# Kernel tuning notes

Measured on AMD Instinct MI355X. Metric: run time of the kernel, lower is better.

## Reference

```python
import jax, jax.numpy as jnp
import numpy as np

B, N = 1, 768
C_S, C_Z, C_H, H, P_QK, P_V = 384, 128, 16, 12, 4, 8
INF = 100000.0
EPS = 1e-8


def _points(s, w, b, rot, trans, P):
    # PointProjection: linear -> [B,N,H,3,P] -> [B,N,H,P,3] local points,
    # then global = R @ p_local + t (rigid broadcast over heads/points).
    pl = (s @ w + b).reshape(s.shape[0], s.shape[1], H, 3, P)
    pl = jnp.moveaxis(pl, -2, -1)  # [B,N,H,P,3]
    return jnp.einsum('bnij,bnhpj->bnhpi', rot, pl) + trans[:, :, None, None, :]


def setup_inputs():
    key = jax.random.key(0)
    ks = jax.random.split(key, 14)

    def lin(k, fi, fo):
        k1, k2 = jax.random.split(k)
        w = jax.random.normal(k1, (fi, fo), jnp.float32) / np.float32(np.sqrt(fi))
        b = jax.random.normal(k2, (fo,), jnp.float32) * 0.01
        return w, b

    s = jax.random.normal(ks[0], (B, N, C_S), jnp.float32)
    z = jax.random.normal(ks[1], (B, N, N, C_Z), jnp.float32)
    rot = jnp.linalg.qr(jax.random.normal(ks[2], (B, N, 3, 3), jnp.float32))[0]
    trans = jax.random.normal(ks[3], (B, N, 3), jnp.float32)
    mask = jnp.ones((B, N), jnp.float32)

    w_q, b_q = lin(ks[4], C_S, H * C_H)
    w_k, b_k = lin(ks[5], C_S, H * C_H)
    w_v, b_v = lin(ks[6], C_S, H * C_H)
    w_qp, b_qp = lin(ks[7], C_S, H * 3 * P_QK)
    w_kp, b_kp = lin(ks[8], C_S, H * 3 * P_QK)
    w_vp, b_vp = lin(ks[9], C_S, H * 3 * P_V)
    w_b, b_b = lin(ks[10], C_Z, H)
    head_weights = jax.random.normal(ks[11], (H,), jnp.float32) * 0.1
    w_o, b_o = lin(ks[12], H * (C_Z + C_H + 4 * P_V), C_S)

    return dict(s=s, z=z, rot=rot, trans=trans, mask=mask,
                w_q=w_q, b_q=b_q, w_k=w_k, b_k=b_k, w_v=w_v, b_v=b_v,
                w_qp=w_qp, b_qp=b_qp, w_kp=w_kp, b_kp=b_kp, w_vp=w_vp, b_vp=b_vp,
                w_b=w_b, b_b=b_b, head_weights=head_weights, w_o=w_o, b_o=b_o)


def reference(s, z, rot, trans, mask,
              w_q, b_q, w_k, b_k, w_v, b_v,
              w_qp, b_qp, w_kp, b_kp, w_vp, b_vp,
              w_b, b_b, head_weights, w_o, b_o):
    # per-head point weights: sqrt(2 / (9 * P_QK)) * softplus(head_weights)
    pw = np.float32(np.sqrt(2.0 / (9.0 * P_QK))) * jnp.logaddexp(head_weights, 0.0)  # [H]

    q_pts = _points(s, w_qp, b_qp, rot, trans, P_QK)  # [B,N,H,P,3]
    k_pts = _points(s, w_kp, b_kp, rot, trans, P_QK)

    # sum_p ||q_p - k_p||^2 expanded: |q|^2 + |k|^2 - 2 q.k (summed over p,xyz)
    qk_pt = jnp.einsum('bqhpc,bkhpc->bqkh', q_pts, k_pts)
    q2 = jnp.sum(q_pts * q_pts, axis=(-2, -1))  # [B,N,H]
    k2 = jnp.sum(k_pts * k_pts, axis=(-2, -1))
    pt_att = -0.5 * pw * (q2[:, :, None, :] + k2[:, None, :, :] - 2.0 * qk_pt)  # [B,Nq,Nk,H]

    q = (s @ w_q + b_q).reshape(B, N, H, C_H) * np.float32(np.sqrt(1.0 / C_H))
    k = (s @ w_k + b_k).reshape(B, N, H, C_H)
    a = pt_att + jnp.einsum('bqhc,bkhc->bqkh', q, k)
    a = a + (z @ w_b + b_b)  # pair bias [B,Nq,Nk,H]

    sq_mask = mask[:, :, None] * mask[:, None, :]
    a = a + (INF * (sq_mask - 1.0))[..., None]
    a = jax.nn.softmax(a * np.float32(np.sqrt(1.0 / 3.0)), axis=-2)  # softmax over k

    v = (s @ w_v + b_v).reshape(B, N, H, C_H)
    o = jnp.einsum('bqkh,bkhc->bqhc', a, v).reshape(B, N, H * C_H)

    v_pts = _points(s, w_vp, b_vp, rot, trans, P_V)  # [B,N,H,P,3]
    o_pt = jnp.einsum('bqkh,bkhpc->bqhpc', a, v_pts).reshape(B, N, H * P_V, 3)
    # inverse rigid: R^T @ (p - t)
    o_pt = jnp.einsum('bnji,bnpj->bnpi', rot, o_pt - trans[:, :, None, :])  # [B,N,H*P_V,3]
    o_pt_norm = jnp.sqrt(jnp.sum(o_pt * o_pt, axis=-1) + EPS)  # [B,N,H*P_V]

    o_pair = jnp.einsum('bqkh,bqkc->bqhc', a, z).reshape(B, N, H * C_Z)

    cat = jnp.concatenate(
        [o, o_pt[..., 0], o_pt[..., 1], o_pt[..., 2], o_pt_norm, o_pair], axis=-1)
    return cat @ w_o + b_o  # [B,N,C_S]
```

## Files before the change

kernel.cpp:

```cpp
#include <hip/hip_runtime.h>
#include <math.h>

#define NN 768
#define KALL 1152
#define CATD 2112
#define INF_ 100000.0f

__device__ __forceinline__ float4 ld4(const float* p) { return *(const float4*)p; }

__global__ __launch_bounds__(256) void pack_kernel(
    const float* wq, const float* bq, const float* wk, const float* bk,
    const float* wv, const float* bv, const float* wqp, const float* bqp,
    const float* wkp, const float* bkp, const float* wvp, const float* bvp,
    float* Wall, float* ball) {
  int idx = blockIdx.x * 256 + threadIdx.x;
  if (idx >= 385 * KALL) return;
  int kk = idx / KALL, u = idx - kk * KALL;
  const float *w, *b; int col, dim; float sc = 1.f;
  if (u < 192)      { w = wq;  b = bq;  col = u;       dim = 192; sc = 0.25f; }
  else if (u < 384) { w = wk;  b = bk;  col = u - 192; dim = 192; }
  else if (u < 576) { w = wv;  b = bv;  col = u - 384; dim = 192; }
  else if (u < 720) { w = wqp; b = bqp; col = u - 576; dim = 144; }
  else if (u < 864) { w = wkp; b = bkp; col = u - 720; dim = 144; }
  else              { w = wvp; b = bvp; col = u - 864; dim = 288; }
  if (kk < 384) Wall[kk * KALL + u] = sc * w[kk * dim + col];
  else          ball[u] = sc * b[col];
}

__global__ __launch_bounds__(256) void proj_kernel(const float* s, const float* Wall,
                                                   const float* ball, float* proj) {
  int q0 = blockIdx.x * 32, c0 = blockIdx.y * 64;
  int tid = threadIdx.x;
  int qa = q0 + (tid >> 4) * 2, qb = qa + 1;
  int c = c0 + (tid & 15) * 4;
  const float* sa = s + qa * 384;
  const float* sb = s + qb * 384;
  const float* wp = Wall + c;
  float4 acc0 = {0, 0, 0, 0}, acc1 = {0, 0, 0, 0};
#pragma unroll 4
  for (int k = 0; k < 384; k++) {
    float4 w4 = ld4(wp + k * KALL);
    float a0 = sa[k], a1 = sb[k];
    acc0.x += a0 * w4.x; acc0.y += a0 * w4.y; acc0.z += a0 * w4.z; acc0.w += a0 * w4.w;
    acc1.x += a1 * w4.x; acc1.y += a1 * w4.y; acc1.z += a1 * w4.z; acc1.w += a1 * w4.w;
  }
  float4 b4 = ld4(ball + c);
  acc0.x += b4.x; acc0.y += b4.y; acc0.z += b4.z; acc0.w += b4.w;
  acc1.x += b4.x; acc1.y += b4.y; acc1.z += b4.z; acc1.w += b4.w;
  *(float4*)(proj + (size_t)qa * KALL + c) = acc0;
  *(float4*)(proj + (size_t)qb * KALL + c) = acc1;
}

__global__ __launch_bounds__(256) void points_kernel(const float* proj, const float* rot,
                                                     const float* trans, float* qpts, float* kpts,
                                                     float* vpts, float* q2, float* k2) {
  int n = blockIdx.x, tid = threadIdx.x;
  __shared__ float sq[12], sk[12];
  if (tid < 12) { sq[tid] = 0.f; sk[tid] = 0.f; }
  __syncthreads();
  if (tid < 192) {
    const float* R = rot + n * 9;
    const float* T = trans + n * 3;
    const float* pr = proj + (size_t)n * KALL;
    int base, P; float* outp; int h; bool isq = false, isk = false;
    if (tid < 48)      { h = tid >> 2; int p = tid & 3; base = 576 + h * 12; P = 4;
                         outp = qpts + n * 144 + h * 12 + p * 3; base += p; isq = true; }
    else if (tid < 96) { int i = tid - 48; h = i >> 2; int p = i & 3; base = 720 + h * 12; P = 4;
                         outp = kpts + n * 144 + h * 12 + p * 3; base += p; isk = true; }
    else               { int i = tid - 96; h = i >> 3; int p = i & 7; base = 864 + h * 24; P = 8;
                         outp = vpts + n * 288 + h * 24 + p * 3; base += p; }
    float l0 = pr[base], l1 = pr[base + P], l2 = pr[base + 2 * P];
    float g0 = R[0] * l0 + R[1] * l1 + R[2] * l2 + T[0];
    float g1 = R[3] * l0 + R[4] * l1 + R[5] * l2 + T[1];
    float g2 = R[6] * l0 + R[7] * l1 + R[8] * l2 + T[2];
    outp[0] = g0; outp[1] = g1; outp[2] = g2;
    float ns = g0 * g0 + g1 * g1 + g2 * g2;
    if (isq) atomicAdd(&sq[h], ns);
    else if (isk) atomicAdd(&sk[h], ns);
  }
  __syncthreads();
  if (tid < 12) { q2[n * 12 + tid] = sq[tid]; k2[n * 12 + tid] = sk[tid]; }
}

__global__ __launch_bounds__(256) void bias_kernel(const float* z, const float* wb,
                                                   const float* bb, float* abuf) {
  int q = blockIdx.x, k0 = blockIdx.y * 128;
  int tid = threadIdx.x;
  __shared__ float wsm[12 * 128];
  __shared__ float bbs[12];
  for (int i = tid; i < 1536; i += 256) { int hh = i >> 7, c = i & 127; wsm[i] = wb[c * 12 + hh]; }
  if (tid < 12) bbs[tid] = bb[tid];
  __syncthreads();
  int kl = tid & 127, h0 = tid >> 7;
  const float* zp = z + (size_t)(q * NN + k0 + kl) * 128;
  float acc[6] = {0, 0, 0, 0, 0, 0};
  for (int c4 = 0; c4 < 128; c4 += 4) {
    float4 z4 = ld4(zp + c4);
    const float zz[4] = {z4.x, z4.y, z4.z, z4.w};
#pragma unroll
    for (int cc = 0; cc < 4; cc++) {
      float zv = zz[cc];
#pragma unroll
      for (int j = 0; j < 6; j++) acc[j] += zv * wsm[(h0 + 2 * j) * 128 + c4 + cc];
    }
  }
#pragma unroll
  for (int j = 0; j < 6; j++) {
    int hh = h0 + 2 * j;
    abuf[((size_t)q * 12 + hh) * NN + k0 + kl] = acc[j] + bbs[hh];
  }
}

__global__ __launch_bounds__(256) void softmax_kernel(const float* proj, const float* qpts,
                                                      const float* kpts, const float* q2,
                                                      const float* k2, const float* mask,
                                                      const float* hw, float* abuf) {
  int q0 = blockIdx.x * 8, h = blockIdx.y;
  int tid = threadIdx.x;
  __shared__ float qw[8][16], qp[8][12], q2s[8], mq[8], red[4][8], row[8], pws;
  if (tid < 128) qw[tid >> 4][tid & 15] = proj[(size_t)(q0 + (tid >> 4)) * KALL + h * 16 + (tid & 15)];
  else if (tid < 224) { int i = tid - 128; qp[i / 12][i % 12] = qpts[(q0 + i / 12) * 144 + h * 12 + i % 12]; }
  else if (tid < 232) q2s[tid - 224] = q2[(q0 + tid - 224) * 12 + h];
  else if (tid < 240) mq[tid - 232] = mask[q0 + tid - 232];
  else if (tid == 240) {
    float x = hw[h];
    pws = 0.23570226039551584f * (fmaxf(x, 0.f) + log1pf(__expf(-fabsf(x))));
  }
  __syncthreads();

  float L[3][8];
#pragma unroll
  for (int i = 0; i < 3; i++) {
    int kk = i * 256 + tid;
    float kw[16], kp[12];
    const float* kwp = proj + (size_t)kk * KALL + 192 + h * 16;
    *(float4*)(kw) = ld4(kwp); *(float4*)(kw + 4) = ld4(kwp + 4);
    *(float4*)(kw + 8) = ld4(kwp + 8); *(float4*)(kw + 12) = ld4(kwp + 12);
    const float* kpp = kpts + (size_t)kk * 144 + h * 12;
    *(float4*)(kp) = ld4(kpp); *(float4*)(kp + 4) = ld4(kpp + 4); *(float4*)(kp + 8) = ld4(kpp + 8);
    float k2v = k2[kk * 12 + h];
    float mk = mask[kk];
#pragma unroll
    for (int q = 0; q < 8; q++) {
      float d = 0.f, dp = 0.f;
#pragma unroll
      for (int j = 0; j < 16; j++) d += qw[q][j] * kw[j];
#pragma unroll
      for (int j = 0; j < 12; j++) dp += qp[q][j] * kp[j];
      float bias = abuf[((size_t)(q0 + q) * 12 + h) * NN + kk];
      float val = bias + d - 0.5f * pws * (q2s[q] + k2v - 2.f * dp) + INF_ * (mq[q] * mk - 1.f);
      L[i][q] = val * 0.5773502691896258f;
    }
  }
  float m[8];
#pragma unroll
  for (int q = 0; q < 8; q++) m[q] = fmaxf(fmaxf(L[0][q], L[1][q]), L[2][q]);
#pragma unroll
  for (int d = 1; d < 64; d <<= 1)
#pragma unroll
    for (int q = 0; q < 8; q++) m[q] = fmaxf(m[q], __shfl_xor(m[q], d, 64));
  int wv = tid >> 6;
  if ((tid & 63) == 0)
    for (int q = 0; q < 8; q++) red[wv][q] = m[q];
  __syncthreads();
  if (tid < 8) row[tid] = fmaxf(fmaxf(red[0][tid], red[1][tid]), fmaxf(red[2][tid], red[3][tid]));
  __syncthreads();
  float sm[8];
#pragma unroll
  for (int q = 0; q < 8; q++) {
    float mm = row[q];
    L[0][q] = __expf(L[0][q] - mm);
    L[1][q] = __expf(L[1][q] - mm);
    L[2][q] = __expf(L[2][q] - mm);
    sm[q] = L[0][q] + L[1][q] + L[2][q];
  }
#pragma unroll
  for (int d = 1; d < 64; d <<= 1)
#pragma unroll
    for (int q = 0; q < 8; q++) sm[q] += __shfl_xor(sm[q], d, 64);
  if ((tid & 63) == 0)
    for (int q = 0; q < 8; q++) red[wv][q] = sm[q];
  __syncthreads();
  if (tid < 8) row[tid] = 1.f / (red[0][tid] + red[1][tid] + red[2][tid] + red[3][tid]);
  __syncthreads();
#pragma unroll
  for (int q = 0; q < 8; q++) {
    float r = row[q];
    float* ap = abuf + ((size_t)(q0 + q) * 12 + h) * NN + tid;
    ap[0] = L[0][q] * r; ap[256] = L[1][q] * r; ap[512] = L[2][q] * r;
  }
}

__global__ __launch_bounds__(256) void opair_kernel(const float* z, const float* abuf, float* cat) {
  int q = blockIdx.x, tid = threadIdx.x;
  int c = tid & 127, h0 = tid >> 7;
  const float* zp = z + (size_t)q * NN * 128 + c;
  const float* ap = abuf + (size_t)q * 12 * NN;
  float acc[6] = {0, 0, 0, 0, 0, 0};
  for (int k4 = 0; k4 < NN; k4 += 4) {
    float4 av[6];
#pragma unroll
    for (int j = 0; j < 6; j++) av[j] = ld4(ap + (h0 + 2 * j) * NN + k4);
#pragma unroll
    for (int kk = 0; kk < 4; kk++) {
      float zv = zp[(size_t)(k4 + kk) * 128];
      const float* avf;
#pragma unroll
      for (int j = 0; j < 6; j++) {
        avf = (const float*)&av[j];
        acc[j] += zv * avf[kk];
      }
    }
  }
#pragma unroll
  for (int j = 0; j < 6; j++)
    cat[(size_t)q * CATD + 576 + (h0 + 2 * j) * 128 + c] = acc[j];
}

__global__ __launch_bounds__(256) void ov_kernel(const float* proj, const float* vpts,
                                                 const float* abuf, const float* rot,
                                                 const float* trans, float* cat) {
  int h = blockIdx.x, q0 = blockIdx.y * 32;
  int tid = threadIdx.x;
  int qg = tid >> 3, jb = tid & 7;
  int q = q0 + qg;
  const float* ap = abuf + ((size_t)q * 12 + h) * NN;
  const float* vp = proj + 384 + h * 16;
  const float* vpp = vpts + h * 24;
  float acc[5] = {0, 0, 0, 0, 0};
  for (int k = 0; k < NN; k += 4) {
    float4 a4 = ld4(ap + k);
    const float af[4] = {a4.x, a4.y, a4.z, a4.w};
#pragma unroll
    for (int kk = 0; kk < 4; kk++) {
      float av = af[kk];
      size_t kr = k + kk;
      acc[0] += av * vp[kr * KALL + jb];
      acc[1] += av * vp[kr * KALL + jb + 8];
      acc[2] += av * vpp[kr * 288 + jb];
      acc[3] += av * vpp[kr * 288 + jb + 8];
      acc[4] += av * vpp[kr * 288 + jb + 16];
    }
  }
  float* cq = cat + (size_t)q * CATD;
  cq[h * 16 + jb] = acc[0];
  cq[h * 16 + jb + 8] = acc[1];
  __shared__ float g[32][24];
  g[qg][jb] = acc[2]; g[qg][jb + 8] = acc[3]; g[qg][jb + 16] = acc[4];
  __syncthreads();
  int ql = tid >> 3, p = tid & 7;
  int qq = q0 + ql;
  float gx = g[ql][p * 3], gy = g[ql][p * 3 + 1], gz = g[ql][p * 3 + 2];
  const float* R = rot + qq * 9;
  const float* T = trans + qq * 3;
  float dx = gx - T[0], dy = gy - T[1], dz = gz - T[2];
  float lx = R[0] * dx + R[3] * dy + R[6] * dz;
  float ly = R[1] * dx + R[4] * dy + R[7] * dz;
  float lz = R[2] * dx + R[5] * dy + R[8] * dz;
  float nrm = sqrtf(lx * lx + ly * ly + lz * lz + 1e-8f);
  int hp = h * 8 + p;
  float* co = cat + (size_t)qq * CATD;
  co[192 + hp] = lx; co[288 + hp] = ly; co[384 + hp] = lz; co[480 + hp] = nrm;
}

__global__ __launch_bounds__(256) void out_part_kernel(const float* cat, const float* wo,
                                                       float* part) {
  int q0 = blockIdx.x * 16, c0 = blockIdx.y * 64, k0 = blockIdx.z * 264;
  int tid = threadIdx.x;
  int q = q0 + (tid >> 4);
  int c = c0 + (tid & 15) * 4;
  const float* cp = cat + (size_t)q * CATD + k0;
  const float* wp = wo + (size_t)k0 * 384 + c;
  float4 acc = {0, 0, 0, 0};
#pragma unroll 8
  for (int k = 0; k < 264; k++) {
    float a = cp[k];
    float4 w4 = ld4(wp + (size_t)k * 384);
    acc.x += a * w4.x; acc.y += a * w4.y; acc.z += a * w4.z; acc.w += a * w4.w;
  }
  *(float4*)(part + ((size_t)blockIdx.z * 768 + q) * 384 + c) = acc;
}

__global__ __launch_bounds__(256) void out_reduce_kernel(const float* part, const float* bo,
                                                         float* out) {
  int idx = blockIdx.x * 256 + threadIdx.x;
  int q = idx / 96, cg = idx - q * 96;
  int c = cg * 4;
  float4 acc = ld4(bo + c);
#pragma unroll
  for (int j = 0; j < 8; j++) {
    float4 p = ld4(part + ((size_t)j * 768 + q) * 384 + c);
    acc.x += p.x; acc.y += p.y; acc.z += p.z; acc.w += p.w;
  }
  *(float4*)(out + (size_t)q * 384 + c) = acc;
}

extern "C" void kernel_launch(void* const* d_in, const int* in_sizes, int n_in,
                              void* d_out, int out_size, void* d_ws, size_t ws_size,
                              hipStream_t stream) {
  const float* s     = (const float*)d_in[0];
  const float* z     = (const float*)d_in[1];
  const float* rot   = (const float*)d_in[2];
  const float* trans = (const float*)d_in[3];
  const float* mask  = (const float*)d_in[4];
  const float* wq    = (const float*)d_in[5];
  const float* bq    = (const float*)d_in[6];
  const float* wk    = (const float*)d_in[7];
  const float* bk    = (const float*)d_in[8];
  const float* wv    = (const float*)d_in[9];
  const float* bv    = (const float*)d_in[10];
  const float* wqp   = (const float*)d_in[11];
  const float* bqp   = (const float*)d_in[12];
  const float* wkp   = (const float*)d_in[13];
  const float* bkp   = (const float*)d_in[14];
  const float* wvp   = (const float*)d_in[15];
  const float* bvp   = (const float*)d_in[16];
  const float* wb    = (const float*)d_in[17];
  const float* bb    = (const float*)d_in[18];
  const float* hw    = (const float*)d_in[19];
  const float* wo    = (const float*)d_in[20];
  const float* bo    = (const float*)d_in[21];
  float* out = (float*)d_out;

  float* ws = (float*)d_ws;
  float* proj  = ws;
  float* Wall  = proj + 884736;
  float* ball  = Wall + 442368;
  float* qpts  = ball + 1152;
  float* kpts  = qpts + 110592;
  float* vpts  = kpts + 110592;
  float* q2    = vpts + 221184;
  float* k2    = q2 + 9216;
  float* abuf  = k2 + 9216;
  float* cat   = abuf + 7077888;
  float* part  = cat + 1622016;

  pack_kernel<<<dim3((385 * KALL + 255) / 256), 256, 0, stream>>>(
      wq, bq, wk, bk, wv, bv, wqp, bqp, wkp, bkp, wvp, bvp, Wall, ball);
  proj_kernel<<<dim3(24, 18), 256, 0, stream>>>(s, Wall, ball, proj);
  points_kernel<<<dim3(768), 256, 0, stream>>>(proj, rot, trans, qpts, kpts, vpts, q2, k2);
  bias_kernel<<<dim3(768, 6), 256, 0, stream>>>(z, wb, bb, abuf);
  softmax_kernel<<<dim3(96, 12), 256, 0, stream>>>(proj, qpts, kpts, q2, k2, mask, hw, abuf);
  opair_kernel<<<dim3(768), 256, 0, stream>>>(z, abuf, cat);
  ov_kernel<<<dim3(12, 24), 256, 0, stream>>>(proj, vpts, abuf, rot, trans, cat);
  out_part_kernel<<<dim3(48, 6, 8), 256, 0, stream>>>(cat, wo, part);
  out_reduce_kernel<<<dim3(288), 256, 0, stream>>>(part, bo, out);
}
```

Measured before the change: 929.8 us.

## Fuse pair-bias and softmax per query row; restage opair and ov kernels

Merges the pair-bias projection and the logit/softmax computation into one kernel per query row. Logits are held in LDS, so the raw bias no longer makes a round trip through global memory. The opair kernel now stages the attention row in LDS and splits the k range across two halves with a shared-memory reduction. The ov kernel is remapped to float4 accumulators per thread group over 24-query tiles. The fused kernel uses about 40KB of LDS and leaves 64 threads idle during the bias phase, which may reduce occupancy.

Result: slower. 994.1 us (+6.9%).

```diff
diff --git a/kernel.cpp b/kernel.cpp
--- a/kernel.cpp
+++ b/kernel.cpp
@@ -82,185 +82,188 @@
   if (tid < 12) { q2[n * 12 + tid] = sq[tid]; k2[n * 12 + tid] = sk[tid]; }
 }
 
-__global__ __launch_bounds__(256) void bias_kernel(const float* z, const float* wb,
-                                                   const float* bb, float* abuf) {
-  int q = blockIdx.x, k0 = blockIdx.y * 128;
+__global__ __launch_bounds__(256) void attn_kernel(
+    const float* z, const float* wb, const float* bb, const float* proj,
+    const float* qpts, const float* kpts, const float* q2, const float* k2,
+    const float* mask, const float* hw, float* abuf) {
+  int q = blockIdx.x;
   int tid = threadIdx.x;
-  __shared__ float wsm[12 * 128];
-  __shared__ float bbs[12];
-  for (int i = tid; i < 1536; i += 256) { int hh = i >> 7, c = i & 127; wsm[i] = wb[c * 12 + hh]; }
-  if (tid < 12) bbs[tid] = bb[tid];
-  __syncthreads();
-  int kl = tid & 127, h0 = tid >> 7;
-  const float* zp = z + (size_t)(q * NN + k0 + kl) * 128;
-  float acc[6] = {0, 0, 0, 0, 0, 0};
-  for (int c4 = 0; c4 < 128; c4 += 4) {
-    float4 z4 = ld4(zp + c4);
-    const float zz[4] = {z4.x, z4.y, z4.z, z4.w};
-#pragma unroll
-    for (int cc = 0; cc < 4; cc++) {
-      float zv = zz[cc];
-#pragma unroll
-      for (int j = 0; j < 6; j++) acc[j] += zv * wsm[(h0 + 2 * j) * 128 + c4 + cc];
-    }
-  }
-#pragma unroll
-  for (int j = 0; j < 6; j++) {
-    int hh = h0 + 2 * j;
-    abuf[((size_t)q * 12 + hh) * NN + k0 + kl] = acc[j] + bbs[hh];
-  }
-}
-
-__global__ __launch_bounds__(256) void softmax_kernel(const float* proj, const float* qpts,
-                                                      const float* kpts, const float* q2,
-                                                      const float* k2, const float* mask,
-                                                      const float* hw, float* abuf) {
-  int q0 = blockIdx.x * 8, h = blockIdx.y;
-  int tid = threadIdx.x;
-  __shared__ float qw[8][16], qp[8][12], q2s[8], mq[8], red[4][8], row[8], pws;
-  if (tid < 128) qw[tid >> 4][tid & 15] = proj[(size_t)(q0 + (tid >> 4)) * KALL + h * 16 + (tid & 15)];
-  else if (tid < 224) { int i = tid - 128; qp[i / 12][i % 12] = qpts[(q0 + i / 12) * 144 + h * 12 + i % 12]; }
-  else if (tid < 232) q2s[tid - 224] = q2[(q0 + tid - 224) * 12 + h];
-  else if (tid < 240) mq[tid - 232] = mask[q0 + tid - 232];
-  else if (tid == 240) {
-    float x = hw[h];
-    pws = 0.23570226039551584f * (fmaxf(x, 0.f) + log1pf(__expf(-fabsf(x))));
-  }
-  __syncthreads();
-
-  float L[3][8];
-#pragma unroll
-  for (int i = 0; i < 3; i++) {
-    int kk = i * 256 + tid;
-    float kw[16], kp[12];
-    const float* kwp = proj + (size_t)kk * KALL + 192 + h * 16;
-    *(float4*)(kw) = ld4(kwp); *(float4*)(kw + 4) = ld4(kwp + 4);
-    *(float4*)(kw + 8) = ld4(kwp + 8); *(float4*)(kw + 12) = ld4(kwp + 12);
-    const float* kpp = kpts + (size_t)kk * 144 + h * 12;
-    *(float4*)(kp) = ld4(kpp); *(float4*)(kp + 4) = ld4(kpp + 4); *(float4*)(kp + 8) = ld4(kpp + 8);
-    float k2v = k2[kk * 12 + h];
-    float mk = mask[kk];
-#pragma unroll
-    for (int q = 0; q < 8; q++) {
-      float d = 0.f, dp = 0.f;
-#pragma unroll
-      for (int j = 0; j < 16; j++) d += qw[q][j] * kw[j];
-#pragma unroll
-      for (int j = 0; j < 12; j++) dp += qp[q][j] * kp[j];
-      float bias = abuf[((size_t)(q0 + q) * 12 + h) * NN + kk];
-      float val = bias + d - 0.5f * pws * (q2s[q] + k2v - 2.f * dp) + INF_ * (mq[q] * mk - 1.f);
-      L[i][q] = val * 0.5773502691896258f;
-    }
-  }
-  float m[8];
-#pragma unroll
-  for (int q = 0; q < 8; q++) m[q] = fmaxf(fmaxf(L[0][q], L[1][q]), L[2][q]);
-#pragma unroll
-  for (int d = 1; d < 64; d <<= 1)
-#pragma unroll
-    for (int q = 0; q < 8; q++) m[q] = fmaxf(m[q], __shfl_xor(m[q], d, 64));
-  int wv = tid >> 6;
-  if ((tid & 63) == 0)
-    for (int q = 0; q < 8; q++) red[wv][q] = m[q];
-  __syncthreads();
-  if (tid < 8) row[tid] = fmaxf(fmaxf(red[0][tid], red[1][tid]), fmaxf(red[2][tid], red[3][tid]));
-  __syncthreads();
-  float sm[8];
-#pragma unroll
-  for (int q = 0; q < 8; q++) {
-    float mm = row[q];
-    L[0][q] = __expf(L[0][q] - mm);
-    L[1][q] = __expf(L[1][q] - mm);
-    L[2][q] = __expf(L[2][q] - mm);
-    sm[q] = L[0][q] + L[1][q] + L[2][q];
-  }
-#pragma unroll
-  for (int d = 1; d < 64; d <<= 1)
-#pragma unroll
-    for (int q = 0; q < 8; q++) sm[q] += __shfl_xor(sm[q], d, 64);
-  if ((tid & 63) == 0)
-    for (int q = 0; q < 8; q++) red[wv][q] = sm[q];
-  __syncthreads();
-  if (tid < 8) row[tid] = 1.f / (red[0][tid] + red[1][tid] + red[2][tid] + red[3][tid]);
-  __syncthreads();
-#pragma unroll
-  for (int q = 0; q < 8; q++) {
-    float r = row[q];
-    float* ap = abuf + ((size_t)(q0 + q) * 12 + h) * NN + tid;
-    ap[0] = L[0][q] * r; ap[256] = L[1][q] * r; ap[512] = L[2][q] * r;
+  __shared__ float wbt[12][132];
+  __shared__ float qws[192], qps[144];
+  __shared__ float q2s_[12], bbs_[12], pws_[12];
+  __shared__ float mq_s;
+  __shared__ float a_lds[768 * 13];
+
+  for (int i = tid; i < 1536; i += 256) { int h = i >> 7, c = i & 127; wbt[h][c] = wb[c * 12 + h]; }
+  if (tid < 192) qws[tid] = proj[(size_t)q * KALL + tid];
+  if (tid < 144) qps[tid] = qpts[q * 144 + tid];
+  if (tid < 12) {
+    q2s_[tid] = q2[q * 12 + tid];
+    bbs_[tid] = bb[tid];
+    float x = hw[tid];
+    pws_[tid] = 0.23570226039551584f * (fmaxf(x, 0.f) + log1pf(__expf(-fabsf(x))));
+  }
+  if (tid == 12) mq_s = mask[q];
+  __syncthreads();
+
+  if (tid < 192) {
+    int t = tid;
+    float acc[12][4];
+#pragma unroll
+    for (int h = 0; h < 12; h++)
+#pragma unroll
+      for (int r = 0; r < 4; r++) acc[h][r] = 0.f;
+    const float* zr = z + ((size_t)q * NN + t) * 128;
+    for (int c4 = 0; c4 < 128; c4 += 4) {
+      float4 zv[4];
+      zv[0] = ld4(zr + c4);
+      zv[1] = ld4(zr + 192 * 128 + c4);
+      zv[2] = ld4(zr + 384 * 128 + c4);
+      zv[3] = ld4(zr + 576 * 128 + c4);
+#pragma unroll
+      for (int h = 0; h < 12; h++) {
+        float4 w4 = ld4(&wbt[h][c4]);
+#pragma unroll
+        for (int r = 0; r < 4; r++) {
+          acc[h][r] += zv[r].x * w4.x + zv[r].y * w4.y + zv[r].z * w4.z + zv[r].w * w4.w;
+        }
+      }
+    }
+    float mq = mq_s;
+    float mterm[4];
+#pragma unroll
+    for (int r = 0; r < 4; r++) mterm[r] = INF_ * (mq * mask[t + 192 * r] - 1.f);
+    for (int h = 0; h < 12; h++) {
+      float qwh[16], qph[12];
+#pragma unroll
+      for (int j = 0; j < 16; j++) qwh[j] = qws[h * 16 + j];
+#pragma unroll
+      for (int j = 0; j < 12; j++) qph[j] = qps[h * 12 + j];
+      float q2v = q2s_[h], pwv = pws_[h], bbv = bbs_[h];
+#pragma unroll
+      for (int r = 0; r < 4; r++) {
+        int k = t + 192 * r;
+        const float* kwp = proj + (size_t)k * KALL + 192 + h * 16;
+        float4 a0 = ld4(kwp), a1 = ld4(kwp + 4), a2 = ld4(kwp + 8), a3 = ld4(kwp + 12);
+        float dqk = a0.x * qwh[0] + a0.y * qwh[1] + a0.z * qwh[2] + a0.w * qwh[3]
+                  + a1.x * qwh[4] + a1.y * qwh[5] + a1.z * qwh[6] + a1.w * qwh[7]
+                  + a2.x * qwh[8] + a2.y * qwh[9] + a2.z * qwh[10] + a2.w * qwh[11]
+                  + a3.x * qwh[12] + a3.y * qwh[13] + a3.z * qwh[14] + a3.w * qwh[15];
+        const float* kpp = kpts + (size_t)k * 144 + h * 12;
+        float4 p0 = ld4(kpp), p1 = ld4(kpp + 4), p2 = ld4(kpp + 8);
+        float dpt = p0.x * qph[0] + p0.y * qph[1] + p0.z * qph[2] + p0.w * qph[3]
+                  + p1.x * qph[4] + p1.y * qph[5] + p1.z * qph[6] + p1.w * qph[7]
+                  + p2.x * qph[8] + p2.y * qph[9] + p2.z * qph[10] + p2.w * qph[11];
+        float k2v = k2[k * 12 + h];
+        float L = (acc[h][r] + bbv + dqk - 0.5f * pwv * (q2v + k2v - 2.f * dpt) + mterm[r])
+                  * 0.5773502691896258f;
+        a_lds[k * 13 + h] = L;
+      }
+    }
+  }
+  __syncthreads();
+
+  int w = tid >> 6, lane = tid & 63;
+#pragma unroll
+  for (int hh = 0; hh < 3; hh++) {
+    int h = w + 4 * hh;
+    float v[12];
+    float mx = -1e30f;
+#pragma unroll
+    for (int i = 0; i < 12; i++) {
+      v[i] = a_lds[(lane + 64 * i) * 13 + h];
+      mx = fmaxf(mx, v[i]);
+    }
+#pragma unroll
+    for (int d = 1; d < 64; d <<= 1) mx = fmaxf(mx, __shfl_xor(mx, d, 64));
+    float s = 0.f;
+#pragma unroll
+    for (int i = 0; i < 12; i++) { v[i] = __expf(v[i] - mx); s += v[i]; }
+#pragma unroll
+    for (int d = 1; d < 64; d <<= 1) s += __shfl_xor(s, d, 64);
+    float inv = 1.f / s;
+    float* ap = abuf + ((size_t)q * 12 + h) * NN + lane;
+#pragma unroll
+    for (int i = 0; i < 12; i++) ap[64 * i] = v[i] * inv;
   }
 }
 
 __global__ __launch_bounds__(256) void opair_kernel(const float* z, const float* abuf, float* cat) {
   int q = blockIdx.x, tid = threadIdx.x;
-  int c = tid & 127, h0 = tid >> 7;
-  const float* zp = z + (size_t)q * NN * 128 + c;
-  const float* ap = abuf + (size_t)q * 12 * NN;
-  float acc[6] = {0, 0, 0, 0, 0, 0};
-  for (int k4 = 0; k4 < NN; k4 += 4) {
-    float4 av[6];
-#pragma unroll
-    for (int j = 0; j < 6; j++) av[j] = ld4(ap + (h0 + 2 * j) * NN + k4);
-#pragma unroll
-    for (int kk = 0; kk < 4; kk++) {
-      float zv = zp[(size_t)(k4 + kk) * 128];
-      const float* avf;
-#pragma unroll
-      for (int j = 0; j < 6; j++) {
-        avf = (const float*)&av[j];
-        acc[j] += zv * avf[kk];
-      }
-    }
-  }
-#pragma unroll
-  for (int j = 0; j < 6; j++)
-    cat[(size_t)q * CATD + 576 + (h0 + 2 * j) * 128 + c] = acc[j];
+  __shared__ float a_s[9216];
+  __shared__ float red[1536];
+  for (int i = tid; i < 9216; i += 256) a_s[i] = abuf[(size_t)q * 9216 + i];
+  __syncthreads();
+  int c = tid & 127, half = tid >> 7;
+  const float* zc = z + ((size_t)q * NN + half * 384) * 128 + c;
+  float acc[12] = {0, 0, 0, 0, 0, 0, 0, 0, 0, 0, 0, 0};
+  for (int k4 = 0; k4 < 384; k4 += 4) {
+    float z0 = zc[(size_t)(k4 + 0) * 128];
+    float z1 = zc[(size_t)(k4 + 1) * 128];
+    float z2 = zc[(size_t)(k4 + 2) * 128];
+    float z3 = zc[(size_t)(k4 + 3) * 128];
+    int kb = half * 384 + k4;
+#pragma unroll
+    for (int h = 0; h < 12; h++) {
+      float4 a4 = *(const float4*)&a_s[h * NN + kb];
+      acc[h] += a4.x * z0 + a4.y * z1 + a4.z * z2 + a4.w * z3;
+    }
+  }
+  if (half == 1) {
+#pragma unroll
+    for (int h = 0; h < 12; h++) red[h * 128 + c] = acc[h];
+  }
+  __syncthreads();
+  if (half == 0) {
+#pragma unroll
+    for (int h = 0; h < 12; h++)
+      cat[(size_t)q * CATD + 576 + h * 128 + c] = acc[h] + red[h * 128 + c];
+  }
 }
 
 __global__ __launch_bounds__(256) void ov_kernel(const float* proj, const float* vpts,
                                                  const float* abuf, const float* rot,
                                                  const float* trans, float* cat) {
-  int h = blockIdx.x, q0 = blockIdx.y * 32;
+  int h = blockIdx.x, q0 = blockIdx.y * 24;
   int tid = threadIdx.x;
-  int qg = tid >> 3, jb = tid & 7;
-  int q = q0 + qg;
-  const float* ap = abuf + ((size_t)q * 12 + h) * NN;
-  const float* vp = proj + 384 + h * 16;
-  const float* vpp = vpts + h * 24;
-  float acc[5] = {0, 0, 0, 0, 0};
-  for (int k = 0; k < NN; k += 4) {
-    float4 a4 = ld4(ap + k);
-    const float af[4] = {a4.x, a4.y, a4.z, a4.w};
-#pragma unroll
-    for (int kk = 0; kk < 4; kk++) {
-      float av = af[kk];
-      size_t kr = k + kk;
-      acc[0] += av * vp[kr * KALL + jb];
-      acc[1] += av * vp[kr * KALL + jb + 8];
-      acc[2] += av * vpp[kr * 288 + jb];
-      acc[3] += av * vpp[kr * 288 + jb + 8];
-      acc[4] += av * vpp[kr * 288 + jb + 16];
-    }
-  }
-  float* cq = cat + (size_t)q * CATD;
-  cq[h * 16 + jb] = acc[0];
-  cq[h * 16 + jb + 8] = acc[1];
-  __shared__ float g[32][24];
-  g[qg][jb] = acc[2]; g[qg][jb + 8] = acc[3]; g[qg][jb + 16] = acc[4];
-  __syncthreads();
-  int ql = tid >> 3, p = tid & 7;
-  int qq = q0 + ql;
-  float gx = g[ql][p * 3], gy = g[ql][p * 3 + 1], gz = g[ql][p * 3 + 2];
-  const float* R = rot + qq * 9;
-  const float* T = trans + qq * 3;
-  float dx = gx - T[0], dy = gy - T[1], dz = gz - T[2];
-  float lx = R[0] * dx + R[3] * dy + R[6] * dz;
-  float ly = R[1] * dx + R[4] * dy + R[7] * dz;
-  float lz = R[2] * dx + R[5] * dy + R[8] * dz;
-  float nrm = sqrtf(lx * lx + ly * ly + lz * lz + 1e-8f);
-  int hp = h * 8 + p;
-  float* co = cat + (size_t)qq * CATD;
-  co[192 + hp] = lx; co[288 + hp] = ly; co[384 + hp] = lz; co[480 + hp] = nrm;
+  __shared__ float opt[24][24];
+  if (tid < 240) {
+    int ql = tid / 10, g = tid - ql * 10;
+    int q = q0 + ql;
+    const float* ap = abuf + ((size_t)q * 12 + h) * NN;
+    const float* vb;
+    int stride;
+    if (g < 4) { vb = proj + 384 + h * 16 + g * 4; stride = KALL; }
+    else       { vb = vpts + h * 24 + (g - 4) * 4; stride = 288;  }
+    float4 acc = {0, 0, 0, 0};
+#pragma unroll 4
+    for (int k = 0; k < NN; k++) {
+      float av = ap[k];
+      float4 v4 = ld4(vb + (size_t)k * stride);
+      acc.x += av * v4.x; acc.y += av * v4.y; acc.z += av * v4.z; acc.w += av * v4.w;
+    }
+    if (g < 4) {
+      *(float4*)(cat + (size_t)q * CATD + h * 16 + g * 4) = acc;
+    } else {
+      *(float4*)(&opt[ql][(g - 4) * 4]) = acc;
+    }
+  }
+  __syncthreads();
+  if (tid < 192) {
+    int ql = tid >> 3, p = tid & 7;
+    int q = q0 + ql;
+    float gx = opt[ql][p * 3], gy = opt[ql][p * 3 + 1], gz = opt[ql][p * 3 + 2];
+    const float* R = rot + q * 9;
+    const float* T = trans + q * 3;
+    float dx = gx - T[0], dy = gy - T[1], dz = gz - T[2];
+    float lx = R[0] * dx + R[3] * dy + R[6] * dz;
+    float ly = R[1] * dx + R[4] * dy + R[7] * dz;
+    float lz = R[2] * dx + R[5] * dy + R[8] * dz;
+    float nrm = sqrtf(lx * lx + ly * ly + lz * lz + 1e-8f);
+    int hp = h * 8 + p;
+    float* co = cat + (size_t)q * CATD;
+    co[192 + hp] = lx; co[288 + hp] = ly; co[384 + hp] = lz; co[480 + hp] = nrm;
+  }
 }
 
 __global__ __launch_bounds__(256) void out_part_kernel(const float* cat, const float* wo,
@@ -339,10 +342,9 @@
       wq, bq, wk, bk, wv, bv, wqp, bqp, wkp, bkp, wvp, bvp, Wall, ball);
   proj_kernel<<<dim3(24, 18), 256, 0, stream>>>(s, Wall, ball, proj);
   points_kernel<<<dim3(768), 256, 0, stream>>>(proj, rot, trans, qpts, kpts, vpts, q2, k2);
-  bias_kernel<<<dim3(768, 6), 256, 0, stream>>>(z, wb, bb, abuf);
-  softmax_kernel<<<dim3(96, 12), 256, 0, stream>>>(proj, qpts, kpts, q2, k2, mask, hw, abuf);
+  attn_kernel<<<dim3(768), 256, 0, stream>>>(z, wb, bb, proj, qpts, kpts, q2, k2, mask, hw, abuf);
   opair_kernel<<<dim3(768), 256, 0, stream>>>(z, abuf, cat);
-  ov_kernel<<<dim3(12, 24), 256, 0, stream>>>(proj, vpts, abuf, rot, trans, cat);
+  ov_kernel<<<dim3(12, 32), 256, 0, stream>>>(proj, vpts, abuf, rot, trans, cat);
   out_part_kernel<<<dim3(48, 6, 8), 256, 0, stream>>>(cat, wo, part);
   out_reduce_kernel<<<dim3(288), 256, 0, stream>>>(part, bo, out);
 }
```
